# Performance work log

Measured on AMD Instinct MI355X. Metric: run time of the kernel, lower is better.

The kernel has to match this reference:

```python
import jax, jax.numpy as jnp
import numpy as np
import math

NUM_HEADS = 16
D_EMBED = 1024
D_HEAD = D_EMBED // NUM_HEADS


def setup_inputs() -> dict:
    key = jax.random.key(0)
    k1, k2, k3 = jax.random.split(key, 3)
    B, S = 4, 2048
    x = jax.random.normal(k1, (B, S, D_EMBED), dtype=jnp.float32)
    # Kaiming-ish init for the fused QKV and output projections
    scale_in = 1.0 / math.sqrt(D_EMBED)
    in_proj_weight = jax.random.normal(k2, (3 * D_EMBED, D_EMBED), dtype=jnp.float32) * scale_in
    out_proj_weight = jax.random.normal(k3, (D_EMBED, D_EMBED), dtype=jnp.float32) * scale_in
    return {
        "x": x,
        "in_proj_weight": in_proj_weight,
        "out_proj_weight": out_proj_weight,
        "causal_mask": 1,
    }


def reference(x, in_proj_weight, out_proj_weight, causal_mask):
    B, S, D = x.shape
    # fused QKV projection: x @ W_in^T -> [B, S, 3D], then split
    qkv = jnp.einsum("bsd,ed->bse", x, in_proj_weight)
    q, k, v = jnp.split(qkv, 3, axis=-1)
    # [B, S, H, dh] -> [B, H, S, dh]
    def to_heads(t):
        return t.reshape(B, S, NUM_HEADS, D_HEAD).transpose(0, 2, 1, 3)
    q, k, v = to_heads(q), to_heads(k), to_heads(v)
    # scores: [B, H, S, S]
    scores = jnp.einsum("bhqd,bhkd->bhqk", q, k) / math.sqrt(D_HEAD)
    if causal_mask:
        mask = jnp.triu(jnp.ones((S, S), dtype=bool), k=1)
        scores = jnp.where(mask, -jnp.inf, scores)
    attn = jax.nn.softmax(scores, axis=-1)
    out = jnp.einsum("bhqk,bhkd->bhqd", attn, v)
    out = out.transpose(0, 2, 1, 3).reshape(B, S, D)
    return jnp.einsum("bsd,ed->bse", out, out_proj_weight)
```

## Files before the change

kernel.cpp:

```cpp
#include <hip/hip_runtime.h>
#include <hip/hip_bf16.h>
#include <stdint.h>

typedef unsigned short u16;
typedef __attribute__((ext_vector_type(8))) short short8;
typedef __attribute__((ext_vector_type(4))) float floatx4;
typedef __attribute__((ext_vector_type(16))) float floatx16;
typedef __attribute__((ext_vector_type(4))) unsigned uint4v;
typedef __attribute__((ext_vector_type(2))) unsigned uint2v;

#define DEV static __device__ __forceinline__

DEV u16 f2bf(float f) {
  __hip_bfloat16 h = __float2bfloat16(f);
  return __builtin_bit_cast(u16, h);
}

DEV float fexp2(float x) {
  float r;
  asm("v_exp_f32 %0, %1" : "=v"(r) : "v"(x));
  return r;
}

DEV unsigned cvtpk(float lo, float hi) {
  unsigned r;
  asm("v_cvt_pk_bf16_f32 %0, %1, %2" : "=v"(r) : "v"(lo), "v"(hi));
  return r;
}

DEV void pswap(unsigned& a, unsigned& b) {
  uint2v r = __builtin_amdgcn_permlane32_swap(a, b, false, false);
  a = r[0];
  b = r[1];
}

DEV void cross32(float v, float& x, float& y) {
  unsigned a = __builtin_bit_cast(unsigned, v), b = a;
  pswap(a, b);
  x = __builtin_bit_cast(float, a);
  y = __builtin_bit_cast(float, b);
}

DEV floatx4 mfma16(short8 a, short8 b, floatx4 c) {
  return __builtin_amdgcn_mfma_f32_16x16x32_bf16(a, b, c, 0, 0, 0);
}
DEV floatx16 mfma32(short8 a, short8 b, floatx16 c) {
  return __builtin_amdgcn_mfma_f32_32x32x16_bf16(a, b, c, 0, 0, 0);
}

DEV void gload_lds16(const void* g, void* l) {
  __builtin_amdgcn_global_load_lds(
      (void __attribute__((address_space(1)))*)(g),
      (void __attribute__((address_space(3)))*)(l),
      16, 0, 0);
}

__global__ void cast_kernel(const float* __restrict__ in, u16* __restrict__ out, int n4) {
  int i = blockIdx.x * 256 + threadIdx.x;
  if (i >= n4) return;
  float4 v = reinterpret_cast<const float4*>(in)[i];
  ushort4 o;
  o.x = f2bf(v.x); o.y = f2bf(v.y); o.z = f2bf(v.z); o.w = f2bf(v.w);
  reinterpret_cast<ushort4*>(out)[i] = o;
}

template <int MODE>
__global__ __launch_bounds__(256, 2)
void gemm_bt(const u16* __restrict__ A, const u16* __restrict__ W,
             int M, int N, int K,
             u16* __restrict__ Qb, u16* __restrict__ Kb, u16* __restrict__ Vb,
             float* __restrict__ C) {
  __shared__ u16 As[128 * 32];
  __shared__ u16 Bs[128 * 32];
  const int tid = threadIdx.x;
  const int wave = tid >> 6, lane = tid & 63;
  const int lr = lane & 15, lg = lane >> 4;
  const int m0 = blockIdx.y * 128, n0 = blockIdx.x * 128;
  const int mq0 = (wave >> 1) * 64, nq0 = (wave & 1) * 64;
  const int srow = lane >> 2;
  const int sk8  = (lane & 3) * 8;

  floatx4 acc[4][4];
#pragma unroll
  for (int i = 0; i < 4; ++i)
#pragma unroll
    for (int j = 0; j < 4; ++j) acc[i][j] = (floatx4)0.f;

  for (int kt = 0; kt < K; kt += 32) {
    __syncthreads();
#pragma unroll
    for (int i = 0; i < 2; ++i) {
      int seg = wave + 4 * i;
      int r = seg * 16 + srow;
      gload_lds16(&A[(size_t)(m0 + r) * K + kt + sk8], &As[seg * 512]);
      gload_lds16(&W[(size_t)(n0 + r) * K + kt + sk8], &Bs[seg * 512]);
    }
    __syncthreads();

    short8 af[4], bf[4];
#pragma unroll
    for (int t = 0; t < 4; ++t)
      af[t] = *reinterpret_cast<const short8*>(&As[(mq0 + t * 16 + lr) * 32 + lg * 8]);
#pragma unroll
    for (int t = 0; t < 4; ++t)
      bf[t] = *reinterpret_cast<const short8*>(&Bs[(nq0 + t * 16 + lr) * 32 + lg * 8]);
#pragma unroll
    for (int i = 0; i < 4; ++i)
#pragma unroll
      for (int j = 0; j < 4; ++j)
        acc[i][j] = mfma16(af[i], bf[j], acc[i][j]);
  }

  if (MODE == 0) {
#pragma unroll
    for (int j = 0; j < 4; ++j) {
      int n = n0 + nq0 + j * 16 + lr;
      int which = n >> 10;
      int d = n & 1023;
      int h = d >> 6, dh = d & 63;
      u16* dst = (which == 0) ? Qb : ((which == 1) ? Kb : Vb);
      float scale = (which == 0) ? 0.18033688f : 1.0f;
#pragma unroll
      for (int i = 0; i < 4; ++i) {
#pragma unroll
        for (int r = 0; r < 4; ++r) {
          int m = m0 + mq0 + i * 16 + lg * 4 + r;
          int b = m >> 11, s = m & 2047;
          dst[((size_t)(b * 16 + h) * 2048 + s) * 64 + dh] = f2bf(acc[i][j][r] * scale);
        }
      }
    }
  } else {
#pragma unroll
    for (int i = 0; i < 4; ++i)
#pragma unroll
      for (int j = 0; j < 4; ++j)
#pragma unroll
        for (int r = 0; r < 4; ++r) {
          int m = m0 + mq0 + i * 16 + lg * 4 + r;
          int n = n0 + nq0 + j * 16 + lr;
          C[(size_t)m * N + n] = acc[i][j][r];
        }
  }
}

__global__ __launch_bounds__(256, 2)
void attn_kernel(const u16* __restrict__ Qb, const u16* __restrict__ Kb,
                 const u16* __restrict__ Vb, u16* __restrict__ Ob) {
  const int bh = blockIdx.y;
  const u16* Qh = Qb + (size_t)bh * 2048 * 64;
  const u16* Kh = Kb + (size_t)bh * 2048 * 64;
  const u16* Vh = Vb + (size_t)bh * 2048 * 64;

  __shared__ u16 smem[8192];
  u16* Ks = smem;
  u16* Vt = smem + 4096;

  const int tid = threadIdx.x, wave = tid >> 6, lane = tid & 63;
  const int ln31 = lane & 31, hi = lane >> 5;
  const int swz = (lane & 7) * 8;
  const int b = bh >> 4, h = bh & 15;

  const int vp = tid & 31, vc8 = tid >> 5;

  for (int ph = 0; ph < 2; ++ph) {
    const int tq = ph ? (15 - (int)blockIdx.x) : (int)blockIdx.x;
    const int q0w = tq * 128 + wave * 32;
    const int qrow = q0w + ln31;

    short8 qf[4];
#pragma unroll
    for (int c = 0; c < 4; ++c)
      qf[c] = *reinterpret_cast<const short8*>(
          &Qh[(size_t)qrow * 64 + c * 16 + hi * 8]);

    floatx16 accO0 = (floatx16)0.f, accO1 = (floatx16)0.f;
    float m_run = -1e30f, l_run = 0.f;

    const int nt = 2 * (tq + 1);
    for (int t = 0; t < nt; ++t) {
      const int kv0 = t * 64;
      __syncthreads();
#pragma unroll
      for (int i = 0; i < 2; ++i) {
        int s = i * 256 + tid;
        int row = s >> 3;
        int col = ((s & 7) ^ (row & 7)) * 8;
        gload_lds16(&Kh[(size_t)(kv0 + row) * 64 + col], &Ks[(size_t)s * 8]);
      }
      {
        short8 v0 = *reinterpret_cast<const short8*>(&Vh[(size_t)(kv0 + 2 * vp) * 64 + vc8 * 8]);
        short8 v1 = *reinterpret_cast<const short8*>(&Vh[(size_t)(kv0 + 2 * vp + 1) * 64 + vc8 * 8]);
#pragma unroll
        for (int j = 0; j < 8; ++j) {
          int d = vc8 * 8 + j;
          uint32_t pk = (uint32_t)(u16)v0[j] | ((uint32_t)(u16)v1[j] << 16);
          *reinterpret_cast<uint32_t*>(&Vt[d * 64 + ((2 * vp) ^ ((d & 7) * 8))]) = pk;
        }
      }
      __syncthreads();

      if (kv0 <= q0w + 31) {
        floatx16 S0 = (floatx16)0.f, S1 = (floatx16)0.f;
        __builtin_amdgcn_s_setprio(1);
#pragma unroll
        for (int c = 0; c < 4; ++c) {
          short8 kfA = *reinterpret_cast<const short8*>(
              &Ks[ln31 * 64 + ((c * 16 + hi * 8) ^ swz)]);
          short8 kfB = *reinterpret_cast<const short8*>(
              &Ks[(32 + ln31) * 64 + ((c * 16 + hi * 8) ^ swz)]);
          S0 = mfma32(kfA, qf[c], S0);
          S1 = mfma32(kfB, qf[c], S1);
        }
        __builtin_amdgcn_s_setprio(0);
        if (kv0 + 63 > q0w) {
#pragma unroll
          for (int reg = 0; reg < 16; ++reg) {
            int kvA = kv0 + (reg & 3) + 8 * (reg >> 2) + 4 * hi;
            if (kvA > qrow) S0[reg] = -1e30f;
            if (kvA + 32 > qrow) S1[reg] = -1e30f;
          }
        }
        float m8[8];
#pragma unroll
        for (int i = 0; i < 8; ++i)
          m8[i] = fmaxf(fmaxf(S0[i], S0[i + 8]), fmaxf(S1[i], S1[i + 8]));
        float mx = fmaxf(fmaxf(fmaxf(m8[0], m8[1]), fmaxf(m8[2], m8[3])),
                         fmaxf(fmaxf(m8[4], m8[5]), fmaxf(m8[6], m8[7])));
        {
          float xa, xb;
          cross32(mx, xa, xb);
          mx = fmaxf(xa, xb);
        }
        bool small_ = (mx <= m_run + 8.f);
        if (!__all(small_)) {
          float mn = fmaxf(m_run, mx);
          float fac = fexp2(m_run - mn);
          m_run = mn;
          l_run *= fac;
          accO0 *= fac;
          accO1 *= fac;
        }
#pragma unroll
        for (int i = 0; i < 16; ++i) S0[i] = fexp2(S0[i] - m_run);
#pragma unroll
        for (int i = 0; i < 16; ++i) S1[i] = fexp2(S1[i] - m_run);
        float a8[8];
#pragma unroll
        for (int i = 0; i < 8; ++i)
          a8[i] = (S0[i] + S0[i + 8]) + (S1[i] + S1[i + 8]);
        float rs = ((a8[0] + a8[1]) + (a8[2] + a8[3])) + ((a8[4] + a8[5]) + (a8[6] + a8[7]));
        {
          float xa, xb;
          cross32(rs, xa, xb);
          rs = xa + xb;
        }
        l_run += rs;
        short8 pf[4];
#define BUILD_PF(idx, S, base)                                        \
        {                                                             \
          unsigned u01 = cvtpk(S[base + 0], S[base + 1]);             \
          unsigned u23 = cvtpk(S[base + 2], S[base + 3]);             \
          unsigned u45 = cvtpk(S[base + 4], S[base + 5]);             \
          unsigned u67 = cvtpk(S[base + 6], S[base + 7]);             \
          pswap(u01, u45);                                            \
          pswap(u23, u67);                                            \
          uint4v w; w.x = u01; w.y = u23; w.z = u45; w.w = u67;       \
          pf[idx] = __builtin_bit_cast(short8, w);                    \
        }
        BUILD_PF(0, S0, 0)
        BUILD_PF(1, S0, 8)
        BUILD_PF(2, S1, 0)
        BUILD_PF(3, S1, 8)
#undef BUILD_PF
        __builtin_amdgcn_s_setprio(1);
#pragma unroll
        for (int c = 0; c < 4; ++c) {
          short8 vfA = *reinterpret_cast<const short8*>(
              &Vt[ln31 * 64 + ((c * 16 + hi * 8) ^ swz)]);
          short8 vfB = *reinterpret_cast<const short8*>(
              &Vt[(32 + ln31) * 64 + ((c * 16 + hi * 8) ^ swz)]);
          accO0 = mfma32(vfA, pf[c], accO0);
          accO1 = mfma32(vfB, pf[c], accO1);
        }
        __builtin_amdgcn_s_setprio(0);
      }
    }

    __syncthreads();
    u16* ep = smem + wave * 2048;
    float inv = 1.0f / l_run;
#define EPI_W(ACC, dh2)                                               \
    {                                                                 \
      _Pragma("unroll")                                               \
      for (int rp = 0; rp < 8; ++rp) {                                \
        int reg = rp * 2;                                             \
        unsigned pk = cvtpk(ACC[reg] * inv, ACC[reg + 1] * inv);      \
        int d = dh2 * 32 + (reg & 3) + 8 * (reg >> 2) + 4 * hi;       \
        *reinterpret_cast<uint32_t*>(                                 \
            &ep[ln31 * 64 + (d ^ ((ln31 & 7) * 8))]) = pk;            \
      }                                                               \
    }
    EPI_W(accO0, 0)
    EPI_W(accO1, 1)
#undef EPI_W
#pragma unroll
    for (int g = 0; g < 4; ++g) {
      int d0 = hi * 32 + g * 8;
      short8 o8 = *reinterpret_cast<const short8*>(
          &ep[ln31 * 64 + (d0 ^ ((ln31 & 7) * 8))]);
      *reinterpret_cast<short8*>(
          &Ob[(size_t)(b * 2048 + q0w + ln31) * 1024 + h * 64 + d0]) = o8;
    }
  }
}

extern "C" void kernel_launch(void* const* d_in, const int* in_sizes, int n_in,
                              void* d_out, int out_size, void* d_ws, size_t ws_size,
                              hipStream_t stream) {
  const float* x    = (const float*)d_in[0];
  const float* win  = (const float*)d_in[1];
  const float* wout = (const float*)d_in[2];
  float* out = (float*)d_out;

  char* ws = (char*)d_ws;
  u16* xb    = (u16*)(ws + 0);
  u16* winb  = (u16*)(ws + 16777216);
  u16* woutb = (u16*)(ws + 23068672);
  u16* Qb    = (u16*)(ws + 25165824);
  u16* Kb    = (u16*)(ws + 41943040);
  u16* Vb    = (u16*)(ws + 58720256);
  u16* Ob    = (u16*)(ws + 75497472);

  cast_kernel<<<8192, 256, 0, stream>>>(x, xb, 2097152);
  cast_kernel<<<3072, 256, 0, stream>>>(win, winb, 786432);
  cast_kernel<<<1024, 256, 0, stream>>>(wout, woutb, 262144);

  gemm_bt<0><<<dim3(24, 64), 256, 0, stream>>>(xb, winb, 8192, 3072, 1024,
                                               Qb, Kb, Vb, nullptr);
  attn_kernel<<<dim3(8, 64), 256, 0, stream>>>(Qb, Kb, Vb, Ob);
  gemm_bt<1><<<dim3(8, 64), 256, 0, stream>>>(Ob, woutb, 8192, 1024, 1024,
                                              nullptr, nullptr, nullptr, out);
}
```

Baseline: 184.1 us.

## Double-buffer LDS tiles in GEMM and attention kernels to overlap loads

Both the projection GEMM and the attention kernel now keep two LDS buffers. The next K-slice or KV tile is prefetched into one buffer while MFMAs consume the other, which removes one barrier per iteration and hides global-load latency. In the attention kernel the V transpose is staged in registers during compute and written to LDS afterwards. This doubles LDS use, to 32KB per block in attention, and raises register pressure, which may reduce occupancy. Correctness depends on the async LDS load completing before the single barrier at the end of each iteration.

```diff
diff --git a/kernel.cpp b/kernel.cpp
--- a/kernel.cpp
+++ b/kernel.cpp
@@ -70,8 +70,8 @@
              int M, int N, int K,
              u16* __restrict__ Qb, u16* __restrict__ Kb, u16* __restrict__ Vb,
              float* __restrict__ C) {
-  __shared__ u16 As[128 * 32];
-  __shared__ u16 Bs[128 * 32];
+  __shared__ u16 As[2][128 * 32];
+  __shared__ u16 Bs[2][128 * 32];
   const int tid = threadIdx.x;
   const int wave = tid >> 6, lane = tid & 63;
   const int lr = lane & 15, lg = lane >> 4;
@@ -86,29 +86,42 @@
 #pragma unroll
     for (int j = 0; j < 4; ++j) acc[i][j] = (floatx4)0.f;
 
+#pragma unroll
+  for (int i = 0; i < 2; ++i) {
+    int seg = wave + 4 * i;
+    int r = seg * 16 + srow;
+    gload_lds16(&A[(size_t)(m0 + r) * K + sk8], &As[0][seg * 512]);
+    gload_lds16(&W[(size_t)(n0 + r) * K + sk8], &Bs[0][seg * 512]);
+  }
+  __syncthreads();
+
+  int cur = 0;
   for (int kt = 0; kt < K; kt += 32) {
-    __syncthreads();
-#pragma unroll
-    for (int i = 0; i < 2; ++i) {
-      int seg = wave + 4 * i;
-      int r = seg * 16 + srow;
-      gload_lds16(&A[(size_t)(m0 + r) * K + kt + sk8], &As[seg * 512]);
-      gload_lds16(&W[(size_t)(n0 + r) * K + kt + sk8], &Bs[seg * 512]);
-    }
-    __syncthreads();
+    if (kt + 32 < K) {
+#pragma unroll
+      for (int i = 0; i < 2; ++i) {
+        int seg = wave + 4 * i;
+        int r = seg * 16 + srow;
+        gload_lds16(&A[(size_t)(m0 + r) * K + kt + 32 + sk8], &As[cur ^ 1][seg * 512]);
+        gload_lds16(&W[(size_t)(n0 + r) * K + kt + 32 + sk8], &Bs[cur ^ 1][seg * 512]);
+      }
+    }
 
     short8 af[4], bf[4];
 #pragma unroll
     for (int t = 0; t < 4; ++t)
-      af[t] = *reinterpret_cast<const short8*>(&As[(mq0 + t * 16 + lr) * 32 + lg * 8]);
+      af[t] = *reinterpret_cast<const short8*>(&As[cur][(mq0 + t * 16 + lr) * 32 + lg * 8]);
 #pragma unroll
     for (int t = 0; t < 4; ++t)
-      bf[t] = *reinterpret_cast<const short8*>(&Bs[(nq0 + t * 16 + lr) * 32 + lg * 8]);
+      bf[t] = *reinterpret_cast<const short8*>(&Bs[cur][(nq0 + t * 16 + lr) * 32 + lg * 8]);
 #pragma unroll
     for (int i = 0; i < 4; ++i)
 #pragma unroll
       for (int j = 0; j < 4; ++j)
         acc[i][j] = mfma16(af[i], bf[j], acc[i][j]);
+
+    __syncthreads();
+    cur ^= 1;
   }
 
   if (MODE == 0) {
@@ -152,9 +165,7 @@
   const u16* Kh = Kb + (size_t)bh * 2048 * 64;
   const u16* Vh = Vb + (size_t)bh * 2048 * 64;
 
-  __shared__ u16 smem[8192];
-  u16* Ks = smem;
-  u16* Vt = smem + 4096;
+  __shared__ u16 smem[2][8192];
 
   const int tid = threadIdx.x, wave = tid >> 6, lane = tid & 63;
   const int ln31 = lane & 31, hi = lane >> 5;
@@ -178,27 +189,48 @@
     float m_run = -1e30f, l_run = 0.f;
 
     const int nt = 2 * (tq + 1);
+
+    __syncthreads();
+#pragma unroll
+    for (int i = 0; i < 2; ++i) {
+      int s = i * 256 + tid;
+      int row = s >> 3;
+      int col = ((s & 7) ^ (row & 7)) * 8;
+      gload_lds16(&Kh[(size_t)row * 64 + col], &smem[0][(size_t)s * 8]);
+    }
+    {
+      short8 v0 = *reinterpret_cast<const short8*>(&Vh[(size_t)(2 * vp) * 64 + vc8 * 8]);
+      short8 v1 = *reinterpret_cast<const short8*>(&Vh[(size_t)(2 * vp + 1) * 64 + vc8 * 8]);
+#pragma unroll
+      for (int j = 0; j < 8; ++j) {
+        int d = vc8 * 8 + j;
+        uint32_t pk = (uint32_t)(u16)v0[j] | ((uint32_t)(u16)v1[j] << 16);
+        *reinterpret_cast<uint32_t*>(&smem[0][4096 + d * 64 + ((2 * vp) ^ ((d & 7) * 8))]) = pk;
+      }
+    }
+    __syncthreads();
+
+    int cur = 0;
     for (int t = 0; t < nt; ++t) {
       const int kv0 = t * 64;
-      __syncthreads();
-#pragma unroll
-      for (int i = 0; i < 2; ++i) {
-        int s = i * 256 + tid;
-        int row = s >> 3;
-        int col = ((s & 7) ^ (row & 7)) * 8;
-        gload_lds16(&Kh[(size_t)(kv0 + row) * 64 + col], &Ks[(size_t)s * 8]);
-      }
-      {
-        short8 v0 = *reinterpret_cast<const short8*>(&Vh[(size_t)(kv0 + 2 * vp) * 64 + vc8 * 8]);
-        short8 v1 = *reinterpret_cast<const short8*>(&Vh[(size_t)(kv0 + 2 * vp + 1) * 64 + vc8 * 8]);
-#pragma unroll
-        for (int j = 0; j < 8; ++j) {
-          int d = vc8 * 8 + j;
-          uint32_t pk = (uint32_t)(u16)v0[j] | ((uint32_t)(u16)v1[j] << 16);
-          *reinterpret_cast<uint32_t*>(&Vt[d * 64 + ((2 * vp) ^ ((d & 7) * 8))]) = pk;
-        }
-      }
-      __syncthreads();
+      const bool have_next = (t + 1 < nt);
+
+      short8 nv0, nv1;
+      if (have_next) {
+        const int kvn = kv0 + 64;
+#pragma unroll
+        for (int i = 0; i < 2; ++i) {
+          int s = i * 256 + tid;
+          int row = s >> 3;
+          int col = ((s & 7) ^ (row & 7)) * 8;
+          gload_lds16(&Kh[(size_t)(kvn + row) * 64 + col], &smem[cur ^ 1][(size_t)s * 8]);
+        }
+        nv0 = *reinterpret_cast<const short8*>(&Vh[(size_t)(kvn + 2 * vp) * 64 + vc8 * 8]);
+        nv1 = *reinterpret_cast<const short8*>(&Vh[(size_t)(kvn + 2 * vp + 1) * 64 + vc8 * 8]);
+      }
+
+      const u16* Ks = smem[cur];
+      const u16* Vt = smem[cur] + 4096;
 
       if (kv0 <= q0w + 31) {
         floatx16 S0 = (floatx16)0.f, S1 = (floatx16)0.f;
@@ -285,10 +317,21 @@
         }
         __builtin_amdgcn_s_setprio(0);
       }
-    }
-
-    __syncthreads();
-    u16* ep = smem + wave * 2048;
+
+      if (have_next) {
+#pragma unroll
+        for (int j = 0; j < 8; ++j) {
+          int d = vc8 * 8 + j;
+          uint32_t pk = (uint32_t)(u16)nv0[j] | ((uint32_t)(u16)nv1[j] << 16);
+          *reinterpret_cast<uint32_t*>(
+              &smem[cur ^ 1][4096 + d * 64 + ((2 * vp) ^ ((d & 7) * 8))]) = pk;
+        }
+      }
+      __syncthreads();
+      cur ^= 1;
+    }
+
+    u16* ep = &smem[0][0] + wave * 2048;
     float inv = 1.0f / l_run;
 #define EPI_W(ACC, dh2)                                               \
     {                                                                 \
```

New measurement: 185.2 us. Within noise of the previous version (+0.6%).
